# Kernel tuning notes

Hardware: AMD Instinct MI355X
Metric: run time of the kernel (lower is better)

Reference implementation:

```python
import jax, jax.numpy as jnp
import numpy as np

SCALE = 64 ** (-0.5)  # dim_head**-0.5; heads/dim_head otherwise unused in forward


def setup_inputs() -> dict:
    key = jax.random.key(0)
    ks = jax.random.split(key, 7)
    B, C, T = 8, 512, 4096
    s = C ** (-0.5)  # conv1d default init scale-ish
    x = jax.random.normal(ks[0], (B, C, T), dtype=jnp.float32)
    Wq = jax.random.normal(ks[1], (C, C), dtype=jnp.float32) * s
    bq = jax.random.normal(ks[2], (C,), dtype=jnp.float32) * s
    Wk = jax.random.normal(ks[3], (C, C), dtype=jnp.float32) * s
    bk = jax.random.normal(ks[4], (C,), dtype=jnp.float32) * s
    Wv = jax.random.normal(ks[5], (C, C), dtype=jnp.float32) * s
    bv = jax.random.normal(ks[6], (C,), dtype=jnp.float32) * s
    return {"x": x, "Wq": Wq, "bq": bq, "Wk": Wk, "bk": bk, "Wv": Wv, "bv": bv}


def reference(x, Wq, bq, Wk, bk, Wv, bv):
    # 1x1 Conv1d == per-timestep linear over channels: (o,c) x (b,c,t) -> (b,o,t)
    q = jnp.einsum('oc,bct->bot', Wq, x) + bq[None, :, None]
    k = jnp.einsum('oc,bct->bot', Wk, x) + bk[None, :, None]
    v = jnp.einsum('oc,bct->bot', Wv, x) + bv[None, :, None]
    # Channel-channel attention: dots (b, C, C); softmax over last (channel) axis
    dots = jnp.einsum('bct,bdt->bcd', q, k) * SCALE
    attn = jax.nn.softmax(dots, axis=-1)
    # (b,C,C) x (b,C,t) -> (b,C,t); dropout p=0 and to_out unused in original forward
    out = jnp.einsum('bcd,bdt->bct', attn, v)
    return out
```

## Files before the change

### kernel.cpp

```cpp
#include <hip/hip_runtime.h>

#define B_ 8
#define C_ 512
#define T_ 4096

typedef __attribute__((ext_vector_type(8))) __bf16 bf16x8;
typedef __attribute__((ext_vector_type(8))) _Float16 f16x8;
typedef __attribute__((ext_vector_type(8))) unsigned short u16x8;
typedef __attribute__((ext_vector_type(4))) float f32x4;

__device__ __forceinline__ unsigned short f2bf(float f) {
  unsigned int u = __float_as_uint(f);
  u += 0x7fffu + ((u >> 16) & 1u);
  return (unsigned short)(u >> 16);
}
__device__ __forceinline__ float bf2f(unsigned short h) {
  return __uint_as_float(((unsigned int)h) << 16);
}
__device__ __forceinline__ unsigned short f2h(float f) {
  return __builtin_bit_cast(unsigned short, (_Float16)f);
}

__device__ __forceinline__ void async16(unsigned short* ldsdst, const unsigned short* gsrc) {
  __builtin_amdgcn_global_load_lds(
      (__attribute__((address_space(1))) void*)(void*)const_cast<unsigned short*>(gsrc),
      (__attribute__((address_space(3))) void*)(void*)ldsdst,
      16, 0, 0);
}

template <bool F16>
__device__ __forceinline__ f32x4 mfma16(u16x8 a, u16x8 b, f32x4 c) {
  if constexpr (F16)
    return __builtin_amdgcn_mfma_f32_16x16x32_f16(
        __builtin_bit_cast(f16x8, a), __builtin_bit_cast(f16x8, b), c, 0, 0, 0);
  else
    return __builtin_amdgcn_mfma_f32_16x16x32_bf16(
        __builtin_bit_cast(bf16x8, a), __builtin_bit_cast(bf16x8, b), c, 0, 0, 0);
}

struct GemmP {
  const unsigned short* Ah; const unsigned short* Al; long sA; int lda;
  const unsigned short* Bh; const unsigned short* Bl; long sB; int ldb;
  float* Cf; unsigned short* Ch; unsigned short* Cl; long sC; int ldc;
  int kspan; int zparts;
  const float* rowv; const float* colv; const float* bq; const float* bk;
  float scale; float tconst;
};

enum { EPI_F32 = 0, EPI_SPLIT = 1, EPI_F16 = 2, EPI_DOTS = 3, EPI_OUT = 4 };

template <int BM, int BN, bool SA, bool SB, int EPI, bool F16>
__global__ __launch_bounds__(256) void gemm_nt(GemmP g) {
  constexpr int KC = 32;
  constexpr int ASZ = BM * KC, BSZ = BN * KC;
  __shared__ alignas(16) unsigned short lds[(SA ? 2 : 1) * ASZ + (SB ? 2 : 1) * BSZ];
  unsigned short* ldsAh = lds;
  unsigned short* ldsAl = lds + ASZ;
  unsigned short* ldsBh = lds + (SA ? 2 : 1) * ASZ;
  unsigned short* ldsBl = ldsBh + BSZ;

  const int tid = threadIdx.x;
  const int lane = tid & 63, wid = tid >> 6;
  const int wm = wid >> 1, wn = wid & 1;
  constexpr int WM = BM / 2, WN = BN / 2, MF = WM / 16, NF = WN / 16;

  const int bm = blockIdx.x, bn = blockIdx.y, z = blockIdx.z;
  const int b = z / g.zparts, kp = z - b * g.zparts;

  const unsigned short* Ah = g.Ah + (size_t)b * g.sA + (size_t)kp * g.kspan;
  const unsigned short* Al = SA ? (g.Al + (size_t)b * g.sA + (size_t)kp * g.kspan) : nullptr;
  const unsigned short* Bh = g.Bh + (size_t)b * g.sB + (size_t)kp * g.kspan;
  const unsigned short* Bl = SB ? (g.Bl + (size_t)b * g.sB + (size_t)kp * g.kspan) : nullptr;

  f32x4 acc[MF][NF] = {};

  const int kIters = g.kspan / KC;
  for (int kt = 0; kt < kIters; ++kt) {
    const int kb = kt * KC;
#pragma unroll
    for (int r = 0; r < BM / 64; ++r) {
      int idx = tid + r * 256;
      int row = idx >> 2, kc = (idx & 3) << 3;
      size_t goff = (size_t)(bm * BM + row) * g.lda + kb + kc;
      async16(&ldsAh[idx << 3], Ah + goff);
      if constexpr (SA) async16(&ldsAl[idx << 3], Al + goff);
    }
#pragma unroll
    for (int r = 0; r < BN / 64; ++r) {
      int idx = tid + r * 256;
      int row = idx >> 2, kc = (idx & 3) << 3;
      size_t goff = (size_t)(bn * BN + row) * g.ldb + kb + kc;
      async16(&ldsBh[idx << 3], Bh + goff);
      if constexpr (SB) async16(&ldsBl[idx << 3], Bl + goff);
    }
    __syncthreads();

    u16x8 afh[MF], afl[MF], bfh[NF], bfl[NF];
    const int rsel = lane & 15, ksel = (lane >> 4) << 3;
#pragma unroll
    for (int fm = 0; fm < MF; ++fm) {
      int ro = (wm * WM + fm * 16 + rsel) * KC + ksel;
      afh[fm] = *(const u16x8*)&ldsAh[ro];
      if constexpr (SA) afl[fm] = *(const u16x8*)&ldsAl[ro];
    }
#pragma unroll
    for (int fn = 0; fn < NF; ++fn) {
      int ro = (wn * WN + fn * 16 + rsel) * KC + ksel;
      bfh[fn] = *(const u16x8*)&ldsBh[ro];
      if constexpr (SB) bfl[fn] = *(const u16x8*)&ldsBl[ro];
    }
#pragma unroll
    for (int fm = 0; fm < MF; ++fm)
#pragma unroll
      for (int fn = 0; fn < NF; ++fn) {
        acc[fm][fn] = mfma16<F16>(afh[fm], bfh[fn], acc[fm][fn]);
        if constexpr (SB) acc[fm][fn] = mfma16<F16>(afh[fm], bfl[fn], acc[fm][fn]);
        if constexpr (SA) acc[fm][fn] = mfma16<F16>(afl[fm], bfh[fn], acc[fm][fn]);
      }
    __syncthreads();
  }

#pragma unroll
  for (int fm = 0; fm < MF; ++fm)
#pragma unroll
    for (int fn = 0; fn < NF; ++fn)
#pragma unroll
      for (int r = 0; r < 4; ++r) {
        int i = bm * BM + wm * WM + fm * 16 + ((lane >> 4) << 2) + r;
        int j = bn * BN + wn * WN + fn * 16 + (lane & 15);
        float v = acc[fm][fn][r];
        size_t co = (size_t)z * g.sC + (size_t)i * g.ldc + j;
        if constexpr (EPI == EPI_F32) {
          g.Cf[co] = v;
        } else if constexpr (EPI == EPI_SPLIT) {
          unsigned short h = f2bf(v);
          g.Ch[co] = h;
          g.Cl[co] = f2bf(v - bf2f(h));
        } else if constexpr (EPI == EPI_F16) {
          g.Ch[co] = f2h(v);
        } else if constexpr (EPI == EPI_DOTS) {
          float d = g.scale * (v + g.rowv[b * C_ + i] * g.bk[j] +
                               g.bq[i] * (g.colv[b * C_ + j] + g.tconst * g.bk[j]));
          g.Cf[co] = d;
        } else {
          g.Cf[co] = v + g.rowv[b * C_ + i];
        }
      }
}

#define NXB (64 * 8 * 8)
#define PAD 66
__global__ __launch_bounds__(256) void prep_fused(
    const float* __restrict__ x, const float* __restrict__ Wq,
    const float* __restrict__ Wk, const float* __restrict__ Wv,
    unsigned short* __restrict__ Xh, unsigned short* __restrict__ XhT,
    float* __restrict__ S, unsigned short* Wqh, unsigned short* Wql,
    unsigned short* Wkh, unsigned short* Wkl, unsigned short* WvT) {
  __shared__ unsigned short tile[64 * PAD];
  const int tid = threadIdx.x;
  if (blockIdx.x < NXB) {
    const int tl = blockIdx.x;
    const int t0 = (tl & 63) << 6, c0 = ((tl >> 6) & 7) << 6, b = tl >> 9;
    const float* xin = x + ((size_t)(b * C_ + c0)) * T_ + t0;
    unsigned short* xo = Xh + ((size_t)(b * C_ + c0)) * T_ + t0;
#pragma unroll
    for (int r = 0; r < 4; ++r) {
      int p = tid + r * 256;
      int row = p >> 4, c4 = (p & 15) << 2;
      float4 v = *(const float4*)&xin[(size_t)row * T_ + c4];
      unsigned short h0 = f2h(v.x), h1 = f2h(v.y), h2 = f2h(v.z), h3 = f2h(v.w);
      ushort4 hv; hv.x = h0; hv.y = h1; hv.z = h2; hv.w = h3;
      *(ushort4*)&xo[(size_t)row * T_ + c4] = hv;
      unsigned int lo = (unsigned int)h0 | ((unsigned int)h1 << 16);
      unsigned int hi = (unsigned int)h2 | ((unsigned int)h3 << 16);
      ((unsigned int*)&tile[row * PAD + c4])[0] = lo;
      ((unsigned int*)&tile[row * PAD + c4])[1] = hi;
      float s = v.x + v.y + v.z + v.w;
#pragma unroll
      for (int o = 1; o < 16; o <<= 1) s += __shfl_xor(s, o);
      if ((tid & 15) == 0) atomicAdd(&S[b * C_ + c0 + row], s);
    }
    __syncthreads();
#pragma unroll
    for (int r = 0; r < 2; ++r) {
      int idx = tid + r * 256;
      int trow = idx >> 3, cc = (idx & 7) << 3;
      unsigned short vals[8];
#pragma unroll
      for (int j = 0; j < 8; ++j) vals[j] = tile[(cc + j) * PAD + trow];
      *(uint4*)&XhT[((size_t)b * T_ + t0 + trow) * C_ + c0 + cc] = *(uint4*)vals;
    }
  } else {
    int i = (blockIdx.x - NXB) * 256 + tid;
    float q = Wq[i]; unsigned short qh = f2bf(q); Wqh[i] = qh; Wql[i] = f2bf(q - bf2f(qh));
    float k = Wk[i]; unsigned short kh = f2bf(k); Wkh[i] = kh; Wkl[i] = f2bf(k - bf2f(kh));
    float v = Wv[i]; int d = i >> 9, e = i & 511;
    WvT[(e << 9) + d] = f2h(v);
  }
}

__global__ __launch_bounds__(256) void combine_g(const float* __restrict__ gp,
                                                 unsigned short* __restrict__ gh,
                                                 unsigned short* __restrict__ gl) {
  int i = blockIdx.x * 256 + threadIdx.x;
  int b = i >> 18, w = i & 0x3FFFF;
  const float* base = gp + ((size_t)(b * 4) << 18);
  float v = base[w] + base[(1 << 18) + w] + base[(2 << 18) + w] + base[(3 << 18) + w];
  unsigned short h = f2bf(v);
  gh[i] = h;
  gl[i] = f2bf(v - bf2f(h));
}

__global__ __launch_bounds__(256) void qs_ks(const float* __restrict__ Wq, const float* __restrict__ Wk,
                                             const float* __restrict__ s, float* __restrict__ qs,
                                             float* __restrict__ ks) {
  int lane = threadIdx.x & 63, wid = threadIdx.x >> 6;
  int gi = blockIdx.x * 4 + wid;
  int b = gi >> 9, i = gi & 511;
  const float* sv = s + (b << 9);
  const float* wqr = Wq + (size_t)i * C_;
  const float* wkr = Wk + (size_t)i * C_;
  float aq = 0.f, ak = 0.f;
#pragma unroll
  for (int c = lane; c < C_; c += 64) {
    float sc = sv[c];
    aq += wqr[c] * sc;
    ak += wkr[c] * sc;
  }
#pragma unroll
  for (int o = 32; o > 0; o >>= 1) { aq += __shfl_down(aq, o); ak += __shfl_down(ak, o); }
  if (lane == 0) { qs[gi] = aq; ks[gi] = ak; }
}

__global__ __launch_bounds__(256) void softmax_rows(const float* __restrict__ logits,
                                                    const float* __restrict__ bv,
                                                    unsigned short* __restrict__ attn,
                                                    float* __restrict__ ab) {
  const int row = blockIdx.x;
  const int tid = threadIdx.x, lane = tid & 63, wid = tid >> 6;
  const float* L = logits + (size_t)row * C_;
  float v0 = L[tid], v1 = L[tid + 256];
  __shared__ float red[4];
  float m = fmaxf(v0, v1);
#pragma unroll
  for (int o = 32; o > 0; o >>= 1) m = fmaxf(m, __shfl_down(m, o));
  if (lane == 0) red[wid] = m;
  __syncthreads();
  m = fmaxf(fmaxf(red[0], red[1]), fmaxf(red[2], red[3]));
  __syncthreads();
  float e0 = __expf(v0 - m), e1 = __expf(v1 - m);
  float sum = e0 + e1;
#pragma unroll
  for (int o = 32; o > 0; o >>= 1) sum += __shfl_down(sum, o);
  if (lane == 0) red[wid] = sum;
  __syncthreads();
  sum = red[0] + red[1] + red[2] + red[3];
  float inv = 1.f / sum;
  float a0 = e0 * inv, a1 = e1 * inv;
  unsigned short* ar = attn + (size_t)row * C_;
  ar[tid] = f2h(a0);
  ar[tid + 256] = f2h(a1);
  float abv = a0 * bv[tid] + a1 * bv[tid + 256];
  __syncthreads();
#pragma unroll
  for (int o = 32; o > 0; o >>= 1) abv += __shfl_down(abv, o);
  if (lane == 0) red[wid] = abv;
  __syncthreads();
  if (tid == 0) ab[row] = red[0] + red[1] + red[2] + red[3];
}

extern "C" void kernel_launch(void* const* d_in, const int* in_sizes, int n_in,
                              void* d_out, int out_size, void* d_ws, size_t ws_size,
                              hipStream_t stream) {
  const float* x  = (const float*)d_in[0];
  const float* Wq = (const float*)d_in[1];
  const float* bq = (const float*)d_in[2];
  const float* Wk = (const float*)d_in[3];
  const float* bk = (const float*)d_in[4];
  const float* Wv = (const float*)d_in[5];
  const float* bv = (const float*)d_in[6];
  float* out = (float*)d_out;

  char* ws = (char*)d_ws;
  size_t off = 0;
  auto alloc = [&](size_t bytes) {
    char* p = ws + off;
    off += (bytes + 255) & ~(size_t)255;
    return p;
  };
  const size_t XSZ = (size_t)B_ * C_ * T_;
  const size_t GSZ = (size_t)B_ * C_ * C_;

  unsigned short* Xh  = (unsigned short*)alloc(XSZ * 2);
  unsigned short* XhT = (unsigned short*)alloc(XSZ * 2);
  float* Gpart = (float*)alloc((size_t)4 * GSZ * 4);
  unsigned short* Ph   = (unsigned short*)Gpart;
  unsigned short* Pl   = (unsigned short*)Gpart + GSZ;
  float*          Logits = (float*)((char*)Gpart + GSZ * 4);
  unsigned short* Attn = (unsigned short*)((char*)Gpart + GSZ * 8);
  unsigned short* Mh   = (unsigned short*)((char*)Gpart + GSZ * 10);
  unsigned short* Gh = (unsigned short*)alloc(GSZ * 2);
  unsigned short* Gl = (unsigned short*)alloc(GSZ * 2);
  unsigned short* Wqh = (unsigned short*)alloc((size_t)C_ * C_ * 2);
  unsigned short* Wql = (unsigned short*)alloc((size_t)C_ * C_ * 2);
  unsigned short* Wkh = (unsigned short*)alloc((size_t)C_ * C_ * 2);
  unsigned short* Wkl = (unsigned short*)alloc((size_t)C_ * C_ * 2);
  unsigned short* WvT = (unsigned short*)alloc((size_t)C_ * C_ * 2);
  float* S  = (float*)alloc((size_t)B_ * C_ * 4);
  float* Qs = (float*)alloc((size_t)B_ * C_ * 4);
  float* Ks = (float*)alloc((size_t)B_ * C_ * 4);
  float* Ab = (float*)alloc((size_t)B_ * C_ * 4);

  hipMemsetAsync(S, 0, (size_t)B_ * C_ * 4, stream);
  prep_fused<<<NXB + C_ * C_ / 256, 256, 0, stream>>>(x, Wq, Wk, Wv, Xh, XhT, S,
                                                      Wqh, Wql, Wkh, Wkl, WvT);
  qs_ks<<<B_ * C_ / 4, 256, 0, stream>>>(Wq, Wk, S, Qs, Ks);

  {
    GemmP p = {};
    p.Ah = Xh; p.sA = (long)C_ * T_; p.lda = T_;
    p.Bh = Xh; p.sB = (long)C_ * T_; p.ldb = T_;
    p.Cf = Gpart; p.sC = (long)C_ * C_; p.ldc = C_;
    p.kspan = T_ / 4; p.zparts = 4;
    gemm_nt<128, 128, false, false, EPI_F32, true><<<dim3(4, 4, 32), 256, 0, stream>>>(p);
  }
  combine_g<<<(int)(GSZ / 256), 256, 0, stream>>>(Gpart, Gh, Gl);

  {
    GemmP p = {};
    p.Ah = Wqh; p.Al = Wql; p.sA = 0; p.lda = C_;
    p.Bh = Gh; p.Bl = Gl; p.sB = (long)C_ * C_; p.ldb = C_;
    p.Ch = Ph; p.Cl = Pl; p.sC = (long)C_ * C_; p.ldc = C_;
    p.kspan = C_; p.zparts = 1;
    gemm_nt<64, 64, true, true, EPI_SPLIT, false><<<dim3(8, 8, 8), 256, 0, stream>>>(p);
  }
  {
    GemmP p = {};
    p.Ah = Ph; p.Al = Pl; p.sA = (long)C_ * C_; p.lda = C_;
    p.Bh = Wkh; p.Bl = Wkl; p.sB = 0; p.ldb = C_;
    p.Cf = Logits; p.sC = (long)C_ * C_; p.ldc = C_;
    p.kspan = C_; p.zparts = 1;
    p.rowv = Qs; p.colv = Ks; p.bq = bq; p.bk = bk;
    p.scale = 0.125f; p.tconst = (float)T_;
    gemm_nt<64, 64, true, true, EPI_DOTS, false><<<dim3(8, 8, 8), 256, 0, stream>>>(p);
  }
  softmax_rows<<<B_ * C_, 256, 0, stream>>>(Logits, bv, Attn, Ab);
  {
    GemmP p = {};
    p.Ah = Attn; p.sA = (long)C_ * C_; p.lda = C_;
    p.Bh = WvT; p.sB = 0; p.ldb = C_;
    p.Ch = Mh; p.sC = (long)C_ * C_; p.ldc = C_;
    p.kspan = C_; p.zparts = 1;
    gemm_nt<64, 64, false, false, EPI_F16, true><<<dim3(8, 8, 8), 256, 0, stream>>>(p);
  }
  {
    GemmP p = {};
    p.Ah = Mh; p.sA = (long)C_ * C_; p.lda = C_;
    p.Bh = XhT; p.sB = (long)C_ * T_; p.ldb = C_;
    p.Cf = out; p.sC = (long)C_ * T_; p.ldc = T_;
    p.kspan = C_; p.zparts = 1;
    p.rowv = Ab;
    gemm_nt<128, 128, false, false, EPI_OUT, true><<<dim3(C_ / 128, T_ / 128, B_), 256, 0, stream>>>(p);
  }
  (void)in_sizes; (void)n_in; (void)out_size; (void)ws_size;
}
```

Measured before the change: 281.1 us.

## Generalize GEMM tiling, add LDS-staged epilogue, split-K small GEMMs with fused combine

The GEMM template now takes wave tile and K-chunk sizes as parameters. Its epilogue stages results through LDS so global stores are 128-bit and coalesced. The three 512x512 batched GEMMs use split-K by two, with small combine kernels that produce the split bf16 or f16 operands, and the logits combine is folded into the softmax with the bias terms. The Gram GEMM moves to 512 threads with KC=64, and the output GEMM uses KC=64. This targets low occupancy in the small GEMMs and uncoalesced scalar stores, at the cost of extra launches and partial-sum traffic.

```diff
diff --git a/kernel.cpp b/kernel.cpp
--- a/kernel.cpp
+++ b/kernel.cpp
@@ -41,19 +41,24 @@
 struct GemmP {
   const unsigned short* Ah; const unsigned short* Al; long sA; int lda;
   const unsigned short* Bh; const unsigned short* Bl; long sB; int ldb;
-  float* Cf; unsigned short* Ch; unsigned short* Cl; long sC; int ldc;
+  float* Cf; long sC; int ldc;
   int kspan; int zparts;
-  const float* rowv; const float* colv; const float* bq; const float* bk;
-  float scale; float tconst;
+  const float* rowv;
 };
 
-enum { EPI_F32 = 0, EPI_SPLIT = 1, EPI_F16 = 2, EPI_DOTS = 3, EPI_OUT = 4 };
-
-template <int BM, int BN, bool SA, bool SB, int EPI, bool F16>
-__global__ __launch_bounds__(256) void gemm_nt(GemmP g) {
-  constexpr int KC = 32;
+enum { EPI_F32 = 0, EPI_OUT = 1 };
+
+template <int BM, int BN, int WM, int WN, int KC, bool SA, bool SB, int EPI, bool F16>
+__global__ __launch_bounds__((BM / WM) * (BN / WN) * 64) void gemm_nt(GemmP g) {
+  constexpr int NWAVE = (BM / WM) * (BN / WN);
+  constexpr int NT = NWAVE * 64;
   constexpr int ASZ = BM * KC, BSZ = BN * KC;
-  __shared__ alignas(16) unsigned short lds[(SA ? 2 : 1) * ASZ + (SB ? 2 : 1) * BSZ];
+  constexpr int STAGE = (SA ? 2 : 1) * ASZ + (SB ? 2 : 1) * BSZ;
+  constexpr int EPAD = BN + 4;
+  constexpr int EPIB = 32 * EPAD * 4;
+  constexpr int LDSB = (STAGE * 2 > EPIB) ? STAGE * 2 : EPIB;
+  __shared__ alignas(16) char ldsraw[LDSB];
+  unsigned short* lds = (unsigned short*)ldsraw;
   unsigned short* ldsAh = lds;
   unsigned short* ldsAl = lds + ASZ;
   unsigned short* ldsBh = lds + (SA ? 2 : 1) * ASZ;
@@ -61,8 +66,10 @@
 
   const int tid = threadIdx.x;
   const int lane = tid & 63, wid = tid >> 6;
-  const int wm = wid >> 1, wn = wid & 1;
-  constexpr int WM = BM / 2, WN = BN / 2, MF = WM / 16, NF = WN / 16;
+  constexpr int WNB = BN / WN;
+  const int wm = wid / WNB, wn = wid % WNB;
+  constexpr int MF = WM / 16, NF = WN / 16;
+  constexpr int KCH = KC / 8;
 
   const int bm = blockIdx.x, bn = blockIdx.y, z = blockIdx.z;
   const int b = z / g.zparts, kp = z - b * g.zparts;
@@ -78,74 +85,81 @@
   for (int kt = 0; kt < kIters; ++kt) {
     const int kb = kt * KC;
 #pragma unroll
-    for (int r = 0; r < BM / 64; ++r) {
-      int idx = tid + r * 256;
-      int row = idx >> 2, kc = (idx & 3) << 3;
+    for (int r = 0; r < ASZ / (8 * NT); ++r) {
+      int idx = tid + r * NT;
+      int row = idx / KCH, kc = (idx % KCH) << 3;
       size_t goff = (size_t)(bm * BM + row) * g.lda + kb + kc;
       async16(&ldsAh[idx << 3], Ah + goff);
       if constexpr (SA) async16(&ldsAl[idx << 3], Al + goff);
     }
 #pragma unroll
-    for (int r = 0; r < BN / 64; ++r) {
-      int idx = tid + r * 256;
-      int row = idx >> 2, kc = (idx & 3) << 3;
+    for (int r = 0; r < BSZ / (8 * NT); ++r) {
+      int idx = tid + r * NT;
+      int row = idx / KCH, kc = (idx % KCH) << 3;
       size_t goff = (size_t)(bn * BN + row) * g.ldb + kb + kc;
       async16(&ldsBh[idx << 3], Bh + goff);
       if constexpr (SB) async16(&ldsBl[idx << 3], Bl + goff);
     }
     __syncthreads();
 
-    u16x8 afh[MF], afl[MF], bfh[NF], bfl[NF];
     const int rsel = lane & 15, ksel = (lane >> 4) << 3;
 #pragma unroll
-    for (int fm = 0; fm < MF; ++fm) {
-      int ro = (wm * WM + fm * 16 + rsel) * KC + ksel;
-      afh[fm] = *(const u16x8*)&ldsAh[ro];
-      if constexpr (SA) afl[fm] = *(const u16x8*)&ldsAl[ro];
-    }
-#pragma unroll
-    for (int fn = 0; fn < NF; ++fn) {
-      int ro = (wn * WN + fn * 16 + rsel) * KC + ksel;
-      bfh[fn] = *(const u16x8*)&ldsBh[ro];
-      if constexpr (SB) bfl[fn] = *(const u16x8*)&ldsBl[ro];
-    }
-#pragma unroll
-    for (int fm = 0; fm < MF; ++fm)
+    for (int ks = 0; ks < KC; ks += 32) {
+      u16x8 afh[MF], afl[MF], bfh[NF], bfl[NF];
+#pragma unroll
+      for (int fm = 0; fm < MF; ++fm) {
+        int ro = (wm * WM + fm * 16 + rsel) * KC + ks + ksel;
+        afh[fm] = *(const u16x8*)&ldsAh[ro];
+        if constexpr (SA) afl[fm] = *(const u16x8*)&ldsAl[ro];
+      }
 #pragma unroll
       for (int fn = 0; fn < NF; ++fn) {
-        acc[fm][fn] = mfma16<F16>(afh[fm], bfh[fn], acc[fm][fn]);
-        if constexpr (SB) acc[fm][fn] = mfma16<F16>(afh[fm], bfl[fn], acc[fm][fn]);
-        if constexpr (SA) acc[fm][fn] = mfma16<F16>(afl[fm], bfh[fn], acc[fm][fn]);
+        int ro = (wn * WN + fn * 16 + rsel) * KC + ks + ksel;
+        bfh[fn] = *(const u16x8*)&ldsBh[ro];
+        if constexpr (SB) bfl[fn] = *(const u16x8*)&ldsBl[ro];
       }
+#pragma unroll
+      for (int fm = 0; fm < MF; ++fm)
+#pragma unroll
+        for (int fn = 0; fn < NF; ++fn) {
+          acc[fm][fn] = mfma16<F16>(afh[fm], bfh[fn], acc[fm][fn]);
+          if constexpr (SB) acc[fm][fn] = mfma16<F16>(afh[fm], bfl[fn], acc[fm][fn]);
+          if constexpr (SA) acc[fm][fn] = mfma16<F16>(afl[fm], bfh[fn], acc[fm][fn]);
+        }
+    }
     __syncthreads();
   }
 
-#pragma unroll
-  for (int fm = 0; fm < MF; ++fm)
-#pragma unroll
-    for (int fn = 0; fn < NF; ++fn)
-#pragma unroll
-      for (int r = 0; r < 4; ++r) {
-        int i = bm * BM + wm * WM + fm * 16 + ((lane >> 4) << 2) + r;
-        int j = bn * BN + wn * WN + fn * 16 + (lane & 15);
-        float v = acc[fm][fn][r];
-        size_t co = (size_t)z * g.sC + (size_t)i * g.ldc + j;
-        if constexpr (EPI == EPI_F32) {
-          g.Cf[co] = v;
-        } else if constexpr (EPI == EPI_SPLIT) {
-          unsigned short h = f2bf(v);
-          g.Ch[co] = h;
-          g.Cl[co] = f2bf(v - bf2f(h));
-        } else if constexpr (EPI == EPI_F16) {
-          g.Ch[co] = f2h(v);
-        } else if constexpr (EPI == EPI_DOTS) {
-          float d = g.scale * (v + g.rowv[b * C_ + i] * g.bk[j] +
-                               g.bq[i] * (g.colv[b * C_ + j] + g.tconst * g.bk[j]));
-          g.Cf[co] = d;
-        } else {
-          g.Cf[co] = v + g.rowv[b * C_ + i];
-        }
+  float* eb = (float*)ldsraw;
+#pragma unroll
+  for (int ck = 0; ck < BM / 32; ++ck) {
+    if (wm == (ck * 32) / WM) {
+      const int fm0 = ((ck * 32) % WM) / 16;
+#pragma unroll
+      for (int fi = 0; fi < 2; ++fi) {
+        int fm = fm0 + fi;
+#pragma unroll
+        for (int fn = 0; fn < NF; ++fn)
+#pragma unroll
+          for (int r = 0; r < 4; ++r) {
+            int lrow = fi * 16 + ((lane >> 4) << 2) + r;
+            int col = wn * WN + fn * 16 + (lane & 15);
+            eb[lrow * EPAD + col] = acc[fm][fn][r];
+          }
       }
+    }
+    __syncthreads();
+#pragma unroll
+    for (int it = 0; it < (32 * BN / 4) / NT; ++it) {
+      int idx = it * NT + tid;
+      int row = idx / (BN / 4), c4 = (idx % (BN / 4)) * 4;
+      f32x4 v = *(f32x4*)&eb[row * EPAD + c4];
+      int grow = bm * BM + ck * 32 + row;
+      if constexpr (EPI == EPI_OUT) v = v + g.rowv[b * C_ + grow];
+      *(f32x4*)&g.Cf[(size_t)z * g.sC + (size_t)grow * g.ldc + bn * BN + c4] = v;
+    }
+    __syncthreads();
+  }
 }
 
 #define NXB (64 * 8 * 8)
@@ -204,11 +218,31 @@
                                                  unsigned short* __restrict__ gl) {
   int i = blockIdx.x * 256 + threadIdx.x;
   int b = i >> 18, w = i & 0x3FFFF;
-  const float* base = gp + ((size_t)(b * 4) << 18);
-  float v = base[w] + base[(1 << 18) + w] + base[(2 << 18) + w] + base[(3 << 18) + w];
+  const float* base = gp + ((size_t)b << 20);
+  float v = base[w] + base[w + (1 << 18)] + base[w + 2 * (1 << 18)] + base[w + 3 * (1 << 18)];
   unsigned short h = f2bf(v);
   gh[i] = h;
   gl[i] = f2bf(v - bf2f(h));
+}
+
+__global__ __launch_bounds__(256) void combine_p(const float* __restrict__ pp,
+                                                 unsigned short* __restrict__ ph,
+                                                 unsigned short* __restrict__ pl) {
+  int i = blockIdx.x * 256 + threadIdx.x;
+  int b = i >> 18, w = i & 0x3FFFF;
+  const float* base = pp + ((size_t)b << 19);
+  float v = base[w] + base[w + (1 << 18)];
+  unsigned short h = f2bf(v);
+  ph[i] = h;
+  pl[i] = f2bf(v - bf2f(h));
+}
+
+__global__ __launch_bounds__(256) void combine_m(const float* __restrict__ mp,
+                                                 unsigned short* __restrict__ mh) {
+  int i = blockIdx.x * 256 + threadIdx.x;
+  int b = i >> 18, w = i & 0x3FFFF;
+  const float* base = mp + ((size_t)b << 19);
+  mh[i] = f2h(base[w] + base[w + (1 << 18)]);
 }
 
 __global__ __launch_bounds__(256) void qs_ks(const float* __restrict__ Wq, const float* __restrict__ Wk,
@@ -232,14 +266,20 @@
   if (lane == 0) { qs[gi] = aq; ks[gi] = ak; }
 }
 
-__global__ __launch_bounds__(256) void softmax_rows(const float* __restrict__ logits,
-                                                    const float* __restrict__ bv,
-                                                    unsigned short* __restrict__ attn,
-                                                    float* __restrict__ ab) {
+__global__ __launch_bounds__(256) void combine_softmax(
+    const float* __restrict__ lp, const float* __restrict__ qs,
+    const float* __restrict__ ks, const float* __restrict__ bq,
+    const float* __restrict__ bk, const float* __restrict__ bv,
+    unsigned short* __restrict__ attn, float* __restrict__ ab) {
   const int row = blockIdx.x;
+  const int b = row >> 9, i = row & 511;
   const int tid = threadIdx.x, lane = tid & 63, wid = tid >> 6;
-  const float* L = logits + (size_t)row * C_;
-  float v0 = L[tid], v1 = L[tid + 256];
+  const float* p0 = lp + (((size_t)b << 19)) + ((size_t)i << 9);
+  const float* p1 = p0 + (1 << 18);
+  const float qsi = qs[row], bqi = bq[i];
+  const int j0 = tid, j1 = tid + 256;
+  float v0 = 0.125f * (p0[j0] + p1[j0] + qsi * bk[j0] + bqi * (ks[(b << 9) + j0] + 4096.f * bk[j0]));
+  float v1 = 0.125f * (p0[j1] + p1[j1] + qsi * bk[j1] + bqi * (ks[(b << 9) + j1] + 4096.f * bk[j1]));
   __shared__ float red[4];
   float m = fmaxf(v0, v1);
 #pragma unroll
@@ -258,9 +298,9 @@
   float inv = 1.f / sum;
   float a0 = e0 * inv, a1 = e1 * inv;
   unsigned short* ar = attn + (size_t)row * C_;
-  ar[tid] = f2h(a0);
-  ar[tid + 256] = f2h(a1);
-  float abv = a0 * bv[tid] + a1 * bv[tid + 256];
+  ar[j0] = f2h(a0);
+  ar[j1] = f2h(a1);
+  float abv = a0 * bv[j0] + a1 * bv[j1];
   __syncthreads();
 #pragma unroll
   for (int o = 32; o > 0; o >>= 1) abv += __shfl_down(abv, o);
@@ -291,16 +331,21 @@
   const size_t XSZ = (size_t)B_ * C_ * T_;
   const size_t GSZ = (size_t)B_ * C_ * C_;
 
-  unsigned short* Xh  = (unsigned short*)alloc(XSZ * 2);
+  char* XhR = alloc(XSZ * 2);
+  unsigned short* Xh   = (unsigned short*)XhR;
+  unsigned short* Mh   = (unsigned short*)XhR;
+  unsigned short* Attn = (unsigned short*)(XhR + GSZ * 4);
   unsigned short* XhT = (unsigned short*)alloc(XSZ * 2);
   float* Gpart = (float*)alloc((size_t)4 * GSZ * 4);
-  unsigned short* Ph   = (unsigned short*)Gpart;
-  unsigned short* Pl   = (unsigned short*)Gpart + GSZ;
-  float*          Logits = (float*)((char*)Gpart + GSZ * 4);
-  unsigned short* Attn = (unsigned short*)((char*)Gpart + GSZ * 8);
-  unsigned short* Mh   = (unsigned short*)((char*)Gpart + GSZ * 10);
-  unsigned short* Gh = (unsigned short*)alloc(GSZ * 2);
-  unsigned short* Gl = (unsigned short*)alloc(GSZ * 2);
+  float* Ppart = Gpart;
+  float* Mpart = Gpart;
+  float* Lpart = Gpart + 2 * GSZ;
+  char* GhR = alloc(GSZ * 2);
+  char* GlR = alloc(GSZ * 2);
+  unsigned short* Gh = (unsigned short*)GhR;
+  unsigned short* Gl = (unsigned short*)GlR;
+  unsigned short* Ph = (unsigned short*)GhR;
+  unsigned short* Pl = (unsigned short*)GlR;
   unsigned short* Wqh = (unsigned short*)alloc((size_t)C_ * C_ * 2);
   unsigned short* Wql = (unsigned short*)alloc((size_t)C_ * C_ * 2);
   unsigned short* Wkh = (unsigned short*)alloc((size_t)C_ * C_ * 2);
@@ -322,7 +367,8 @@
     p.Bh = Xh; p.sB = (long)C_ * T_; p.ldb = T_;
     p.Cf = Gpart; p.sC = (long)C_ * C_; p.ldc = C_;
     p.kspan = T_ / 4; p.zparts = 4;
-    gemm_nt<128, 128, false, false, EPI_F32, true><<<dim3(4, 4, 32), 256, 0, stream>>>(p);
+    gemm_nt<128, 128, 32, 64, 64, false, false, EPI_F32, true>
+        <<<dim3(4, 4, 32), 512, 0, stream>>>(p);
   }
   combine_g<<<(int)(GSZ / 256), 256, 0, stream>>>(Gpart, Gh, Gl);
 
@@ -330,29 +376,35 @@
     GemmP p = {};
     p.Ah = Wqh; p.Al = Wql; p.sA = 0; p.lda = C_;
     p.Bh = Gh; p.Bl = Gl; p.sB = (long)C_ * C_; p.ldb = C_;
-    p.Ch = Ph; p.Cl = Pl; p.sC = (long)C_ * C_; p.ldc = C_;
-    p.kspan = C_; p.zparts = 1;
-    gemm_nt<64, 64, true, true, EPI_SPLIT, false><<<dim3(8, 8, 8), 256, 0, stream>>>(p);
-  }
+    p.Cf = Ppart; p.sC = (long)C_ * C_; p.ldc = C_;
+    p.kspan = C_ / 2; p.zparts = 2;
+    gemm_nt<64, 64, 32, 32, 32, true, true, EPI_F32, false>
+        <<<dim3(8, 8, 16), 256, 0, stream>>>(p);
+  }
+  combine_p<<<(int)(GSZ / 256), 256, 0, stream>>>(Ppart, Ph, Pl);
+
   {
     GemmP p = {};
     p.Ah = Ph; p.Al = Pl; p.sA = (long)C_ * C_; p.lda = C_;
     p.Bh = Wkh; p.Bl = Wkl; p.sB = 0; p.ldb = C_;
-    p.Cf = Logits; p.sC = (long)C_ * C_; p.ldc = C_;
-    p.kspan = C_; p.zparts = 1;
-    p.rowv = Qs; p.colv = Ks; p.bq = bq; p.bk = bk;
-    p.scale = 0.125f; p.tconst = (float)T_;
-    gemm_nt<64, 64, true, true, EPI_DOTS, false><<<dim3(8, 8, 8), 256, 0, stream>>>(p);
-  }
-  softmax_rows<<<B_ * C_, 256, 0, stream>>>(Logits, bv, Attn, Ab);
+    p.Cf = Lpart; p.sC = (long)C_ * C_; p.ldc = C_;
+    p.kspan = C_ / 2; p.zparts = 2;
+    gemm_nt<64, 64, 32, 32, 32, true, true, EPI_F32, false>
+        <<<dim3(8, 8, 16), 256, 0, stream>>>(p);
+  }
+  combine_softmax<<<B_ * C_, 256, 0, stream>>>(Lpart, Qs, Ks, bq, bk, bv, Attn, Ab);
+
   {
     GemmP p = {};
     p.Ah = Attn; p.sA = (long)C_ * C_; p.lda = C_;
     p.Bh = WvT; p.sB = 0; p.ldb = C_;
-    p.Ch = Mh; p.sC = (long)C_ * C_; p.ldc = C_;
-    p.kspan = C_; p.zparts = 1;
-    gemm_nt<64, 64, false, false, EPI_F16, true><<<dim3(8, 8, 8), 256, 0, stream>>>(p);
-  }
+    p.Cf = Mpart; p.sC = (long)C_ * C_; p.ldc = C_;
+    p.kspan = C_ / 2; p.zparts = 2;
+    gemm_nt<64, 64, 32, 32, 32, false, false, EPI_F32, true>
+        <<<dim3(8, 8, 16), 256, 0, stream>>>(p);
+  }
+  combine_m<<<(int)(GSZ / 256), 256, 0, stream>>>(Mpart, Mh);
+
   {
     GemmP p = {};
     p.Ah = Mh; p.sA = (long)C_ * C_; p.lda = C_;
@@ -360,7 +412,8 @@
     p.Cf = out; p.sC = (long)C_ * T_; p.ldc = T_;
     p.kspan = C_; p.zparts = 1;
     p.rowv = Ab;
-    gemm_nt<128, 128, false, false, EPI_OUT, true><<<dim3(C_ / 128, T_ / 128, B_), 256, 0, stream>>>(p);
+    gemm_nt<128, 128, 64, 64, 64, false, false, EPI_OUT, true>
+        <<<dim3(C_ / 128, T_ / 128, B_), 256, 0, stream>>>(p);
   }
   (void)in_sizes; (void)n_in; (void)out_size; (void)ws_size;
 }
```

Result: no change. 279.1 us (-0.7%).

## Rework GEMM: KC=64 with XOR-swizzled LDS, 8-wave tiles, LDS-staged vector epilogue

Applied to the files above, without the earlier changes.

The templated GEMM now loads 64-wide K chunks into LDS with an XOR swizzle on the 16-byte slot index, which is meant to reduce LDS bank conflicts on fragment reads and halve the number of barriers per K sweep. The 128x128 GEMMs run with 8 waves of 32x64 per-wave tiles and 512 threads. The float epilogues stage accumulators through LDS, 32 rows at a time, so global stores become coalesced 16-byte vector writes. Scratch buffers no longer alias the Gram partials. The cost is more LDS per block, which may lower occupancy, plus extra barriers in the epilogue.

```diff
diff --git a/kernel.cpp b/kernel.cpp
--- a/kernel.cpp
+++ b/kernel.cpp
@@ -44,16 +44,22 @@
   float* Cf; unsigned short* Ch; unsigned short* Cl; long sC; int ldc;
   int kspan; int zparts;
   const float* rowv; const float* colv; const float* bq; const float* bk;
-  float scale; float tconst;
 };
 
-enum { EPI_F32 = 0, EPI_SPLIT = 1, EPI_F16 = 2, EPI_DOTS = 3, EPI_OUT = 4 };
-
-template <int BM, int BN, bool SA, bool SB, int EPI, bool F16>
-__global__ __launch_bounds__(256) void gemm_nt(GemmP g) {
-  constexpr int KC = 32;
+enum { EPI_F32 = 0, EPI_OUT = 1, EPI_DOTS = 2, EPI_SPLIT = 3, EPI_F16 = 4 };
+
+template <int BM, int BN, int WM, int WN, bool SA, bool SB, int EPI, bool F16>
+__global__ __launch_bounds__((BM / WM) * (BN / WN) * 64) void gemm_nt(GemmP g) {
+  constexpr int KC = 64;
+  constexpr int NWAVE = (BM / WM) * (BN / WN);
+  constexpr int NT = NWAVE * 64;
   constexpr int ASZ = BM * KC, BSZ = BN * KC;
-  __shared__ alignas(16) unsigned short lds[(SA ? 2 : 1) * ASZ + (SB ? 2 : 1) * BSZ];
+  constexpr int STAGE = (SA ? 2 : 1) * ASZ + (SB ? 2 : 1) * BSZ;
+  constexpr int EPAD = BN + 4;
+  constexpr int EPIB = 32 * EPAD * 4;
+  constexpr int LDSB = (STAGE * 2 > EPIB) ? STAGE * 2 : EPIB;
+  __shared__ alignas(16) char ldsraw[LDSB];
+  unsigned short* lds = (unsigned short*)ldsraw;
   unsigned short* ldsAh = lds;
   unsigned short* ldsAl = lds + ASZ;
   unsigned short* ldsBh = lds + (SA ? 2 : 1) * ASZ;
@@ -61,8 +67,9 @@
 
   const int tid = threadIdx.x;
   const int lane = tid & 63, wid = tid >> 6;
-  const int wm = wid >> 1, wn = wid & 1;
-  constexpr int WM = BM / 2, WN = BN / 2, MF = WM / 16, NF = WN / 16;
+  constexpr int WNB = BN / WN;
+  const int wm = wid / WNB, wn = wid % WNB;
+  constexpr int MF = WM / 16, NF = WN / 16;
 
   const int bm = blockIdx.x, bn = blockIdx.y, z = blockIdx.z;
   const int b = z / g.zparts, kp = z - b * g.zparts;
@@ -78,74 +85,112 @@
   for (int kt = 0; kt < kIters; ++kt) {
     const int kb = kt * KC;
 #pragma unroll
-    for (int r = 0; r < BM / 64; ++r) {
-      int idx = tid + r * 256;
-      int row = idx >> 2, kc = (idx & 3) << 3;
+    for (int r = 0; r < ASZ / (8 * NT); ++r) {
+      int idx = tid + r * NT;
+      int row = idx >> 3, sl = idx & 7;
+      int kc = (sl ^ (row & 7)) << 3;
       size_t goff = (size_t)(bm * BM + row) * g.lda + kb + kc;
       async16(&ldsAh[idx << 3], Ah + goff);
       if constexpr (SA) async16(&ldsAl[idx << 3], Al + goff);
     }
 #pragma unroll
-    for (int r = 0; r < BN / 64; ++r) {
-      int idx = tid + r * 256;
-      int row = idx >> 2, kc = (idx & 3) << 3;
+    for (int r = 0; r < BSZ / (8 * NT); ++r) {
+      int idx = tid + r * NT;
+      int row = idx >> 3, sl = idx & 7;
+      int kc = (sl ^ (row & 7)) << 3;
       size_t goff = (size_t)(bn * BN + row) * g.ldb + kb + kc;
       async16(&ldsBh[idx << 3], Bh + goff);
       if constexpr (SB) async16(&ldsBl[idx << 3], Bl + goff);
     }
     __syncthreads();
 
-    u16x8 afh[MF], afl[MF], bfh[NF], bfl[NF];
-    const int rsel = lane & 15, ksel = (lane >> 4) << 3;
-#pragma unroll
-    for (int fm = 0; fm < MF; ++fm) {
-      int ro = (wm * WM + fm * 16 + rsel) * KC + ksel;
-      afh[fm] = *(const u16x8*)&ldsAh[ro];
-      if constexpr (SA) afl[fm] = *(const u16x8*)&ldsAl[ro];
-    }
-#pragma unroll
-    for (int fn = 0; fn < NF; ++fn) {
-      int ro = (wn * WN + fn * 16 + rsel) * KC + ksel;
-      bfh[fn] = *(const u16x8*)&ldsBh[ro];
-      if constexpr (SB) bfl[fn] = *(const u16x8*)&ldsBl[ro];
-    }
+    const int rsel = lane & 15, kq = lane >> 4;
+#pragma unroll
+    for (int ks = 0; ks < KC; ks += 32) {
+      const int chunk = (ks >> 3) + kq;
+      u16x8 afh[MF], afl[MF], bfh[NF], bfl[NF];
+#pragma unroll
+      for (int fm = 0; fm < MF; ++fm) {
+        int row = wm * WM + fm * 16 + rsel;
+        int ro = row * KC + ((chunk ^ (row & 7)) << 3);
+        afh[fm] = *(const u16x8*)&ldsAh[ro];
+        if constexpr (SA) afl[fm] = *(const u16x8*)&ldsAl[ro];
+      }
+#pragma unroll
+      for (int fn = 0; fn < NF; ++fn) {
+        int row = wn * WN + fn * 16 + rsel;
+        int ro = row * KC + ((chunk ^ (row & 7)) << 3);
+        bfh[fn] = *(const u16x8*)&ldsBh[ro];
+        if constexpr (SB) bfl[fn] = *(const u16x8*)&ldsBl[ro];
+      }
+#pragma unroll
+      for (int fm = 0; fm < MF; ++fm)
+#pragma unroll
+        for (int fn = 0; fn < NF; ++fn) {
+          acc[fm][fn] = mfma16<F16>(afh[fm], bfh[fn], acc[fm][fn]);
+          if constexpr (SB) acc[fm][fn] = mfma16<F16>(afh[fm], bfl[fn], acc[fm][fn]);
+          if constexpr (SA) acc[fm][fn] = mfma16<F16>(afl[fm], bfh[fn], acc[fm][fn]);
+        }
+    }
+    __syncthreads();
+  }
+
+  if constexpr (EPI == EPI_SPLIT || EPI == EPI_F16) {
 #pragma unroll
     for (int fm = 0; fm < MF; ++fm)
 #pragma unroll
-      for (int fn = 0; fn < NF; ++fn) {
-        acc[fm][fn] = mfma16<F16>(afh[fm], bfh[fn], acc[fm][fn]);
-        if constexpr (SB) acc[fm][fn] = mfma16<F16>(afh[fm], bfl[fn], acc[fm][fn]);
-        if constexpr (SA) acc[fm][fn] = mfma16<F16>(afl[fm], bfh[fn], acc[fm][fn]);
-      }
-    __syncthreads();
-  }
-
-#pragma unroll
-  for (int fm = 0; fm < MF; ++fm)
-#pragma unroll
-    for (int fn = 0; fn < NF; ++fn)
-#pragma unroll
-      for (int r = 0; r < 4; ++r) {
-        int i = bm * BM + wm * WM + fm * 16 + ((lane >> 4) << 2) + r;
-        int j = bn * BN + wn * WN + fn * 16 + (lane & 15);
-        float v = acc[fm][fn][r];
-        size_t co = (size_t)z * g.sC + (size_t)i * g.ldc + j;
-        if constexpr (EPI == EPI_F32) {
-          g.Cf[co] = v;
-        } else if constexpr (EPI == EPI_SPLIT) {
-          unsigned short h = f2bf(v);
-          g.Ch[co] = h;
-          g.Cl[co] = f2bf(v - bf2f(h));
-        } else if constexpr (EPI == EPI_F16) {
-          g.Ch[co] = f2h(v);
-        } else if constexpr (EPI == EPI_DOTS) {
-          float d = g.scale * (v + g.rowv[b * C_ + i] * g.bk[j] +
-                               g.bq[i] * (g.colv[b * C_ + j] + g.tconst * g.bk[j]));
-          g.Cf[co] = d;
-        } else {
-          g.Cf[co] = v + g.rowv[b * C_ + i];
+      for (int fn = 0; fn < NF; ++fn)
+#pragma unroll
+        for (int r = 0; r < 4; ++r) {
+          int i = bm * BM + wm * WM + fm * 16 + ((lane >> 4) << 2) + r;
+          int j = bn * BN + wn * WN + fn * 16 + (lane & 15);
+          float v = acc[fm][fn][r];
+          size_t co = (size_t)z * g.sC + (size_t)i * g.ldc + j;
+          if constexpr (EPI == EPI_SPLIT) {
+            unsigned short h = f2bf(v);
+            g.Ch[co] = h;
+            g.Cl[co] = f2bf(v - bf2f(h));
+          } else {
+            g.Ch[co] = f2h(v);
+          }
+        }
+  } else {
+    float* eb = (float*)ldsraw;
+#pragma unroll
+    for (int ck = 0; ck < BM / 32; ++ck) {
+      if (wm == ck) {
+#pragma unroll
+        for (int fi = 0; fi < MF; ++fi) {
+#pragma unroll
+          for (int fn = 0; fn < NF; ++fn)
+#pragma unroll
+            for (int r = 0; r < 4; ++r) {
+              int lrow = fi * 16 + ((lane >> 4) << 2) + r;
+              int col = wn * WN + fn * 16 + (lane & 15);
+              eb[lrow * EPAD + col] = acc[fi][fn][r];
+            }
         }
       }
+      __syncthreads();
+#pragma unroll
+      for (int it = 0; it < (32 * BN / 4) / NT; ++it) {
+        int idx = it * NT + tid;
+        int row = idx / (BN / 4), c4 = (idx % (BN / 4)) * 4;
+        f32x4 v = *(f32x4*)&eb[row * EPAD + c4];
+        int grow = bm * BM + ck * 32 + row;
+        int j = bn * BN + c4;
+        if constexpr (EPI == EPI_OUT) v = v + g.rowv[b * C_ + grow];
+        if constexpr (EPI == EPI_DOTS) {
+          f32x4 bkv = *(const f32x4*)&g.bk[j];
+          f32x4 ksv = *(const f32x4*)&g.colv[b * C_ + j];
+          float qsi = g.rowv[b * C_ + grow], bqi = g.bq[grow];
+          v = 0.125f * (v + qsi * bkv + bqi * (ksv + 4096.f * bkv));
+        }
+        *(f32x4*)&g.Cf[(size_t)z * g.sC + (size_t)grow * g.ldc + j] = v;
+      }
+      __syncthreads();
+    }
+  }
 }
 
 #define NXB (64 * 8 * 8)
@@ -204,8 +249,8 @@
                                                  unsigned short* __restrict__ gl) {
   int i = blockIdx.x * 256 + threadIdx.x;
   int b = i >> 18, w = i & 0x3FFFF;
-  const float* base = gp + ((size_t)(b * 4) << 18);
-  float v = base[w] + base[(1 << 18) + w] + base[(2 << 18) + w] + base[(3 << 18) + w];
+  const float* base = gp + ((size_t)b << 20);
+  float v = base[w] + base[w + (1 << 18)] + base[w + 2 * (1 << 18)] + base[w + 3 * (1 << 18)];
   unsigned short h = f2bf(v);
   gh[i] = h;
   gl[i] = f2bf(v - bf2f(h));
@@ -294,13 +339,13 @@
   unsigned short* Xh  = (unsigned short*)alloc(XSZ * 2);
   unsigned short* XhT = (unsigned short*)alloc(XSZ * 2);
   float* Gpart = (float*)alloc((size_t)4 * GSZ * 4);
-  unsigned short* Ph   = (unsigned short*)Gpart;
-  unsigned short* Pl   = (unsigned short*)Gpart + GSZ;
-  float*          Logits = (float*)((char*)Gpart + GSZ * 4);
-  unsigned short* Attn = (unsigned short*)((char*)Gpart + GSZ * 8);
-  unsigned short* Mh   = (unsigned short*)((char*)Gpart + GSZ * 10);
   unsigned short* Gh = (unsigned short*)alloc(GSZ * 2);
   unsigned short* Gl = (unsigned short*)alloc(GSZ * 2);
+  unsigned short* Ph = (unsigned short*)alloc(GSZ * 2);
+  unsigned short* Pl = (unsigned short*)alloc(GSZ * 2);
+  float* Logits = (float*)alloc(GSZ * 4);
+  unsigned short* Attn = (unsigned short*)alloc(GSZ * 2);
+  unsigned short* Mh = (unsigned short*)alloc(GSZ * 2);
   unsigned short* Wqh = (unsigned short*)alloc((size_t)C_ * C_ * 2);
   unsigned short* Wql = (unsigned short*)alloc((size_t)C_ * C_ * 2);
   unsigned short* Wkh = (unsigned short*)alloc((size_t)C_ * C_ * 2);
@@ -322,7 +367,8 @@
     p.Bh = Xh; p.sB = (long)C_ * T_; p.ldb = T_;
     p.Cf = Gpart; p.sC = (long)C_ * C_; p.ldc = C_;
     p.kspan = T_ / 4; p.zparts = 4;
-    gemm_nt<128, 128, false, false, EPI_F32, true><<<dim3(4, 4, 32), 256, 0, stream>>>(p);
+    gemm_nt<128, 128, 32, 64, false, false, EPI_F32, true>
+        <<<dim3(4, 4, 32), 512, 0, stream>>>(p);
   }
   combine_g<<<(int)(GSZ / 256), 256, 0, stream>>>(Gpart, Gh, Gl);
 
@@ -332,7 +378,8 @@
     p.Bh = Gh; p.Bl = Gl; p.sB = (long)C_ * C_; p.ldb = C_;
     p.Ch = Ph; p.Cl = Pl; p.sC = (long)C_ * C_; p.ldc = C_;
     p.kspan = C_; p.zparts = 1;
-    gemm_nt<64, 64, true, true, EPI_SPLIT, false><<<dim3(8, 8, 8), 256, 0, stream>>>(p);
+    gemm_nt<64, 64, 32, 32, true, true, EPI_SPLIT, false>
+        <<<dim3(8, 8, 8), 256, 0, stream>>>(p);
   }
   {
     GemmP p = {};
@@ -341,8 +388,8 @@
     p.Cf = Logits; p.sC = (long)C_ * C_; p.ldc = C_;
     p.kspan = C_; p.zparts = 1;
     p.rowv = Qs; p.colv = Ks; p.bq = bq; p.bk = bk;
-    p.scale = 0.125f; p.tconst = (float)T_;
-    gemm_nt<64, 64, true, true, EPI_DOTS, false><<<dim3(8, 8, 8), 256, 0, stream>>>(p);
+    gemm_nt<64, 64, 32, 32, true, true, EPI_DOTS, false>
+        <<<dim3(8, 8, 8), 256, 0, stream>>>(p);
   }
   softmax_rows<<<B_ * C_, 256, 0, stream>>>(Logits, bv, Attn, Ab);
   {
@@ -351,7 +398,8 @@
     p.Bh = WvT; p.sB = 0; p.ldb = C_;
     p.Ch = Mh; p.sC = (long)C_ * C_; p.ldc = C_;
     p.kspan = C_; p.zparts = 1;
-    gemm_nt<64, 64, false, false, EPI_F16, true><<<dim3(8, 8, 8), 256, 0, stream>>>(p);
+    gemm_nt<64, 64, 32, 32, false, false, EPI_F16, true>
+        <<<dim3(8, 8, 8), 256, 0, stream>>>(p);
   }
   {
     GemmP p = {};
@@ -360,7 +408,8 @@
     p.Cf = out; p.sC = (long)C_ * T_; p.ldc = T_;
     p.kspan = C_; p.zparts = 1;
     p.rowv = Ab;
-    gemm_nt<128, 128, false, false, EPI_OUT, true><<<dim3(C_ / 128, T_ / 128, B_), 256, 0, stream>>>(p);
+    gemm_nt<128, 128, 32, 64, false, false, EPI_OUT, true>
+        <<<dim3(C_ / 128, T_ / 128, B_), 512, 0, stream>>>(p);
   }
   (void)in_sizes; (void)n_in; (void)out_size; (void)ws_size;
 }
```

Result: faster. 255.9 us (-9.0%).
